# Kernel optimization log

Measured on AMD Instinct MI355X. Metric: run time of the kernel, lower is better.

## Reference

```python
import jax, jax.numpy as jnp
import numpy as np

EPS = 1e-3  # keras BatchNormalization default epsilon


def _dwconv_t(y, w):
    # depthwise conv along time (axis 1), SAME padding. y:(B,T,S,G,n), w:(G,n,k)
    k = w.shape[-1]
    T = y.shape[1]
    pl = (k - 1) // 2
    yp = jnp.pad(y, ((0, 0), (pl, k - 1 - pl), (0, 0), (0, 0), (0, 0)))
    return sum(yp[:, j:j + T] * w[..., j] for j in range(k))


def _tc_layer(x, w, b, k3, k5, k7, gamma, beta, mu, var):
    # x:(B,T,S,C); w:(5,G,Cg,nb); b/gamma/beta/mu/var:(5,G,nb); k*:(G,nb,k)
    B, T, S, C = x.shape
    G, nb = w.shape[1], w.shape[-1]
    # global spatial pooling: concat [x, max, mean] along spatial axis -> S+2
    x = jnp.concatenate([x, x.max(axis=2, keepdims=True), x.mean(axis=2, keepdims=True)], axis=2)
    S = S + 2
    xg = x.reshape(B, T, S, G, C // G)
    # 5 grouped 1x1x1 pointwise convs at once
    y = jnp.einsum('btsgc,pgcn->pbtsgn', xg, w) + b[:, None, None, None]
    t0 = y[0]
    t3 = _dwconv_t(y[1], k3)
    t5 = _dwconv_t(y[2], k5)
    t7 = _dwconv_t(y[3], k7)
    # temporal maxpool pool=2 stride=1 SAME (TF pads right)
    t1 = jnp.maximum(y[4], jnp.concatenate([y[4][:, 1:], y[4][:, -1:]], axis=1))
    ts = jnp.stack([t0, t3, t5, t7, t1])  # (5,B,T,S,G,nb)
    scale = gamma[:, None, None, None] / jnp.sqrt(var[:, None, None, None] + EPS)
    ts = (ts - mu[:, None, None, None]) * scale + beta[:, None, None, None]
    # concat branches within each group: (B,T,S,G,5*nb)
    z = jnp.transpose(ts, (1, 2, 3, 4, 0, 5)).reshape(B, T, S, G, 5 * nb)
    z = jax.nn.relu(z)
    # channel shuffle: (G, per) -> (per, G) -> flatten
    z = jnp.swapaxes(z, -1, -2).reshape(B, T, S, G * 5 * nb)
    # MaxPooling3D pool=(2,1,1) stride 2 valid: halve T
    return jnp.maximum(z[:, 0::2], z[:, 1::2])


def setup_inputs() -> dict:
    key = jax.random.key(0)
    ks = jax.random.split(key, 32)
    B, T, H, W, C = 16, 64, 7, 7, 1024
    G = 8
    d = {'x': jax.random.normal(ks[0], (B, T, H, W, C), jnp.float32)}
    specs = [(0, 128, 32), (1, 160, 40)]  # (layer, Cg, nb)
    i = 1
    for l, cg, nb in specs:
        d[f'w{l}'] = 0.02 * jax.random.normal(ks[i], (5, G, cg, nb)); i += 1
        d[f'b{l}'] = 0.02 * jax.random.normal(ks[i], (5, G, nb)); i += 1
        d[f'k3_{l}'] = 0.1 * jax.random.normal(ks[i], (G, nb, 3)); i += 1
        d[f'k5_{l}'] = 0.1 * jax.random.normal(ks[i], (G, nb, 5)); i += 1
        d[f'k7_{l}'] = 0.1 * jax.random.normal(ks[i], (G, nb, 7)); i += 1
        d[f'g{l}'] = jax.random.uniform(ks[i], (5, G, nb), minval=0.5, maxval=1.5); i += 1
        d[f'be{l}'] = 0.02 * jax.random.normal(ks[i], (5, G, nb)); i += 1
        d[f'mu{l}'] = 0.02 * jax.random.normal(ks[i], (5, G, nb)); i += 1
        d[f'v{l}'] = jax.random.uniform(ks[i], (5, G, nb), minval=0.5, maxval=1.5); i += 1
    return d


def reference(x, w0, b0, k3_0, k5_0, k7_0, g0, be0, mu0, v0,
              w1, b1, k3_1, k5_1, k7_1, g1, be1, mu1, v1):
    B, T, H, W, C = x.shape
    z = x.reshape(B, T, H * W, C)  # (B,T,S,C), side_dim2=1 kept implicit
    z = _tc_layer(z, w0, b0, k3_0, k5_0, k7_0, g0, be0, mu0, v0)
    z = _tc_layer(z, w1, b1, k3_1, k5_1, k7_1, g1, be1, mu1, v1)
    return z[:, :, :, None, :]  # (B, T/4, S+4, 1, Cout)
```

## Files before the change

kernel.cpp:

```cpp
#include <hip/hip_runtime.h>
#include <hip/hip_bf16.h>

#define EPSBN 1e-3f

typedef __attribute__((ext_vector_type(8))) short bf16x8;
typedef __attribute__((ext_vector_type(8))) unsigned short ushort8;
typedef __attribute__((ext_vector_type(4))) float f32x4;


__device__ __forceinline__ float bf2f(unsigned short u) {
    union { unsigned int i; float f; } c; c.i = (unsigned int)u << 16; return c.f;
}
__device__ __forceinline__ unsigned short f2bf(float f) {
    union { float f; unsigned int i; } c; c.f = f;
    unsigned int r = c.i + 0x7FFF + ((c.i >> 16) & 1);
    return (unsigned short)(r >> 16);
}

__global__ __launch_bounds__(256) void tc_prep(const float* __restrict__ w0,
                                               const float* __restrict__ w1,
                                               unsigned short* __restrict__ W0t,
                                               unsigned short* __restrict__ W1t) {
    const int idx = blockIdx.x * 256 + threadIdx.x;
    if (idx < 163840) {
        const int g   = idx / 20480;
        const int rem = idx - g*20480;
        const int n   = rem >> 7;
        const int k   = rem & 127;
        const int p   = n >> 5, nn = n & 31;
        W0t[idx] = f2bf(w0[(((size_t)p*8 + g)*128 + k)*32 + nn]);
    } else if (idx < 163840 + 256000) {
        const int i2  = idx - 163840;
        const int g   = i2 / 32000;
        const int rem = i2 - g*32000;
        const int n   = rem / 160;
        const int k   = rem - n*160;
        const int kref = (k % 20)*8 + k/20;
        const int p   = n / 40, nn = n - p*40;
        W1t[i2] = f2bf(w1[(((size_t)p*8 + g)*160 + kref)*40 + nn]);
    }
}

__global__ __launch_bounds__(256) void tc_reduce0(const float* __restrict__ x,
                                                  unsigned short* __restrict__ xb,
                                                  unsigned short* __restrict__ extb,
                                                  const int big) {
    const int bt = blockIdx.x;
    const int b  = bt >> 6, t = bt & 63;
    const int c  = threadIdx.x * 4;
    const float4* src = reinterpret_cast<const float4*>(x + (size_t)bt * 49 * 1024 + c);
    float4 v = src[0];
    float mx0 = v.x, mx1 = v.y, mx2 = v.z, mx3 = v.w;
    float sm0 = v.x, sm1 = v.y, sm2 = v.z, sm3 = v.w;
    if (big) {
        ushort4 o; o.x=f2bf(v.x); o.y=f2bf(v.y); o.z=f2bf(v.z); o.w=f2bf(v.w);
        *reinterpret_cast<ushort4*>(&xb[((size_t)(b*51)*64 + t)*1024 + c]) = o;
    }
    for (int s = 1; s < 49; ++s) {
        float4 u = src[(size_t)s * 256];
        mx0 = fmaxf(mx0, u.x); sm0 += u.x;
        mx1 = fmaxf(mx1, u.y); sm1 += u.y;
        mx2 = fmaxf(mx2, u.z); sm2 += u.z;
        mx3 = fmaxf(mx3, u.w); sm3 += u.w;
        if (big) {
            ushort4 o; o.x=f2bf(u.x); o.y=f2bf(u.y); o.z=f2bf(u.z); o.w=f2bf(u.w);
            *reinterpret_cast<ushort4*>(&xb[((size_t)(b*51 + s)*64 + t)*1024 + c]) = o;
        }
    }
    const float inv = 1.0f / 49.0f;
    ushort4 omx, omn;
    omx.x=f2bf(mx0); omx.y=f2bf(mx1); omx.z=f2bf(mx2); omx.w=f2bf(mx3);
    omn.x=f2bf(sm0*inv); omn.y=f2bf(sm1*inv); omn.z=f2bf(sm2*inv); omn.w=f2bf(sm3*inv);
    if (big) {
        *reinterpret_cast<ushort4*>(&xb[((size_t)(b*51 + 49)*64 + t)*1024 + c]) = omx;
        *reinterpret_cast<ushort4*>(&xb[((size_t)(b*51 + 50)*64 + t)*1024 + c]) = omn;
    } else {
        *reinterpret_cast<ushort4*>(&extb[((size_t)(b*2 + 0)*64 + t)*1024 + c]) = omx;
        *reinterpret_cast<ushort4*>(&extb[((size_t)(b*2 + 1)*64 + t)*1024 + c]) = omn;
    }
}

template<int BIG>
__global__ __launch_bounds__(512, 6) void tc_layer0(
    const float* __restrict__ x, const unsigned short* __restrict__ xb,
    const unsigned short* __restrict__ extb,
    const unsigned short* __restrict__ W0t, const float* __restrict__ bias,
    const float* __restrict__ k3, const float* __restrict__ k5,
    const float* __restrict__ k7,
    const float* __restrict__ gam, const float* __restrict__ bet,
    const float* __restrict__ mu, const float* __restrict__ var,
    unsigned short* __restrict__ zb)
{
    const int tid = threadIdx.x;
    const int g   = blockIdx.x / 416;
    const int rem = blockIdx.x % 416;
    const int sp  = rem % 26;
    const int b   = rem / 26;
    const int s0  = sp*2;
    const int has1 = (s0 + 1 < 51);

    __shared__ __align__(16) unsigned short lds[128*136 + 160*40];
    unsigned short* AtU = lds;
    unsigned short* WtU = lds + 128*136;
    unsigned short* Ytb = lds;

    #pragma unroll
    for (int it = 0; it < 4; ++it) {
        const int fid = tid + it*512;
        const int row = fid >> 4;
        const int ch8 = (fid & 15) * 8;
        const int t   = row & 63;
        const int s   = (row < 64) ? s0 : (has1 ? s0+1 : s0);
        ushort8 u;
        if (BIG) {
            u = *reinterpret_cast<const ushort8*>(
                &xb[((size_t)(b*51 + s)*64 + t)*1024 + g*128 + ch8]);
        } else if (s < 49) {
            const float* sp_ = x + ((size_t)(b*64 + t)*49 + s)*1024 + g*128 + ch8;
            const float4 f0 = *reinterpret_cast<const float4*>(sp_);
            const float4 f1 = *reinterpret_cast<const float4*>(sp_ + 4);
            u[0]=f2bf(f0.x); u[1]=f2bf(f0.y); u[2]=f2bf(f0.z); u[3]=f2bf(f0.w);
            u[4]=f2bf(f1.x); u[5]=f2bf(f1.y); u[6]=f2bf(f1.z); u[7]=f2bf(f1.w);
        } else {
            u = *reinterpret_cast<const ushort8*>(
                &extb[((size_t)(b*2 + (s-49))*64 + t)*1024 + g*128 + ch8]);
        }
        *reinterpret_cast<ushort8*>(&AtU[row*136 + ch8]) = u;
    }

    const int lane = tid & 63;
    const int wid  = tid >> 6;
    const int fr   = lane & 15;
    const int kb   = lane >> 4;

    f32x4 zero = {0.f, 0.f, 0.f, 0.f};
    f32x4 acc[10];
    #pragma unroll
    for (int i = 0; i < 10; ++i) acc[i] = zero;

    for (int kc = 0; kc < 4; ++kc) {
        __syncthreads();
        #pragma unroll
        for (int it = 0; it < 2; ++it) {
            const int gi = tid + it*512;
            if (gi < 640) {
                const int n = gi >> 2, part = (gi & 3) * 8;
                *reinterpret_cast<ushort8*>(&WtU[n*40 + part]) =
                    *reinterpret_cast<const ushort8*>(
                        &W0t[((size_t)g*160 + n)*128 + kc*32 + part]);
            }
        }
        __syncthreads();
        const bf16x8 bfrag = *reinterpret_cast<const bf16x8*>(
            &AtU[(wid*16 + fr)*136 + kc*32 + kb*8]);
        #pragma unroll
        for (int nt = 0; nt < 10; ++nt) {
            const bf16x8 afrag = *reinterpret_cast<const bf16x8*>(
                &WtU[(nt*16 + fr)*40 + kb*8]);
            acc[nt] = __builtin_amdgcn_mfma_f32_16x16x32_bf16(afrag, bfrag, acc[nt], 0, 0, 0);
        }
    }
    __syncthreads();
    #pragma unroll
    for (int nt = 0; nt < 10; ++nt)
        #pragma unroll
        for (int r = 0; r < 4; ++r)
            Ytb[(nt*16 + kb*4 + r)*134 + wid*16 + fr] = f2bf(acc[nt][r]);
    __syncthreads();

    if (tid < 320) {
        const int sIdx = (tid >= 160) ? 1 : 0;
        const int ch   = tid - sIdx*160;
        if (!sIdx || has1) {
            const int s  = s0 + sIdx;
            const int p  = ch >> 5, n = ch & 31;
            const int pi = (p*8 + g)*32 + n;
            const float bsv = bias[pi];
            const float sc  = gam[pi]*rsqrtf(var[pi]+EPSBN);
            const float sh  = bet[pi] - mu[pi]*sc;
            float yv[64];
            #pragma unroll
            for (int i = 0; i < 32; ++i) {
                const unsigned int w2 = *reinterpret_cast<const unsigned int*>(
                    &Ytb[ch*134 + sIdx*64 + i*2]);
                yv[2*i]   = bf2f((unsigned short)(w2 & 0xffffu)) + bsv;
                yv[2*i+1] = bf2f((unsigned short)(w2 >> 16)) + bsv;
            }
            unsigned short* zp = zb + ((size_t)(b*32)*53 + s)*1280 + g*160 + ch;
            if (p == 0) {
                #pragma unroll
                for (int tq = 0; tq < 32; ++tq) {
                    const float r = fmaxf(fmaxf(fmaf(yv[2*tq],sc,sh), fmaf(yv[2*tq+1],sc,sh)), 0.f);
                    zp[(size_t)tq*67840] = f2bf(r);
                }
            } else if (p == 1) {
                const float w0_ = k3[(g*32+n)*3+0], w1_ = k3[(g*32+n)*3+1], w2_ = k3[(g*32+n)*3+2];
                #pragma unroll
                for (int tq = 0; tq < 32; ++tq) {
                    float a = yv[2*tq]*w1_;
                    if (tq > 0) a = fmaf(yv[2*tq-1], w0_, a);
                    a = fmaf(yv[2*tq+1], w2_, a);
                    float c2 = fmaf(yv[2*tq], w0_, yv[2*tq+1]*w1_);
                    if (tq < 31) c2 = fmaf(yv[2*tq+2], w2_, c2);
                    const float r = fmaxf(fmaxf(fmaf(a,sc,sh), fmaf(c2,sc,sh)), 0.f);
                    zp[(size_t)tq*67840] = f2bf(r);
                }
            } else if (p == 2) {
                float wk[5];
                #pragma unroll
                for (int j = 0; j < 5; ++j) wk[j] = k5[(g*32+n)*5+j];
                #pragma unroll
                for (int tq = 0; tq < 32; ++tq) {
                    float vv[2];
                    #pragma unroll
                    for (int q = 0; q < 2; ++q) {
                        const int t = 2*tq + q;
                        float v = 0.f;
                        #pragma unroll
                        for (int j = 0; j < 5; ++j) {
                            const int ttp = t + j - 2;
                            if (ttp >= 0 && ttp < 64) v = fmaf(yv[ttp], wk[j], v);
                        }
                        vv[q] = v;
                    }
                    const float r = fmaxf(fmaxf(fmaf(vv[0],sc,sh), fmaf(vv[1],sc,sh)), 0.f);
                    zp[(size_t)tq*67840] = f2bf(r);
                }
            } else if (p == 3) {
                float wk[7];
                #pragma unroll
                for (int j = 0; j < 7; ++j) wk[j] = k7[(g*32+n)*7+j];
                #pragma unroll
                for (int tq = 0; tq < 32; ++tq) {
                    float vv[2];
                    #pragma unroll
                    for (int q = 0; q < 2; ++q) {
                        const int t = 2*tq + q;
                        float v = 0.f;
                        #pragma unroll
                        for (int j = 0; j < 7; ++j) {
                            const int ttp = t + j - 3;
                            if (ttp >= 0 && ttp < 64) v = fmaf(yv[ttp], wk[j], v);
                        }
                        vv[q] = v;
                    }
                    const float r = fmaxf(fmaxf(fmaf(vv[0],sc,sh), fmaf(vv[1],sc,sh)), 0.f);
                    zp[(size_t)tq*67840] = f2bf(r);
                }
            } else {
                #pragma unroll
                for (int tq = 0; tq < 32; ++tq) {
                    const float v0 = fmaxf(yv[2*tq], yv[2*tq+1]);
                    const float v1 = fmaxf(yv[2*tq+1], yv[(2*tq+2 < 64) ? 2*tq+2 : 63]);
                    const float r = fmaxf(fmaxf(fmaf(v0,sc,sh), fmaf(v1,sc,sh)), 0.f);
                    zp[(size_t)tq*67840] = f2bf(r);
                }
            }
        }
    }
}

__global__ __launch_bounds__(320) void tc_reduce1(unsigned short* __restrict__ zb) {
    const int bt = blockIdx.x;
    const int c  = threadIdx.x * 4;
    unsigned short* base = zb + (size_t)bt * 67840;
    ushort4 u = *reinterpret_cast<const ushort4*>(&base[c]);
    float v0 = bf2f(u.x), v1 = bf2f(u.y), v2 = bf2f(u.z), v3 = bf2f(u.w);
    float mx0 = v0, mx1 = v1, mx2 = v2, mx3 = v3;
    float sm0 = v0, sm1 = v1, sm2 = v2, sm3 = v3;
    for (int s = 1; s < 51; ++s) {
        ushort4 w = *reinterpret_cast<const ushort4*>(&base[(size_t)s*1280 + c]);
        v0 = bf2f(w.x); v1 = bf2f(w.y); v2 = bf2f(w.z); v3 = bf2f(w.w);
        mx0 = fmaxf(mx0, v0); sm0 += v0;
        mx1 = fmaxf(mx1, v1); sm1 += v1;
        mx2 = fmaxf(mx2, v2); sm2 += v2;
        mx3 = fmaxf(mx3, v3); sm3 += v3;
    }
    const float inv = 1.0f / 51.0f;
    ushort4 o;
    o.x = f2bf(mx0); o.y = f2bf(mx1); o.z = f2bf(mx2); o.w = f2bf(mx3);
    *reinterpret_cast<ushort4*>(&base[(size_t)51*1280 + c]) = o;
    o.x = f2bf(sm0*inv); o.y = f2bf(sm1*inv); o.z = f2bf(sm2*inv); o.w = f2bf(sm3*inv);
    *reinterpret_cast<ushort4*>(&base[(size_t)52*1280 + c]) = o;
}

__global__ __launch_bounds__(256, 4) void tc_layer1(
    const unsigned short* __restrict__ zbi,
    const unsigned short* __restrict__ W1t, const float* __restrict__ bias,
    const float* __restrict__ k3, const float* __restrict__ k5,
    const float* __restrict__ k7,
    const float* __restrict__ gam, const float* __restrict__ bet,
    const float* __restrict__ mu, const float* __restrict__ var,
    unsigned short* __restrict__ og)
{
    const int tid = threadIdx.x;
    const int g   = blockIdx.x / 432;
    const int rem = blockIdx.x % 432;
    const int sp  = rem % 27;
    const int b   = rem / 27;
    const int s0  = sp*2;
    const int has1 = (s0 + 1 < 53);

    __shared__ __align__(16) unsigned short lds[64*168 + 208*40];
    unsigned short* AtU = lds;
    unsigned short* WtU = lds + 64*168;
    unsigned short* Ytb = lds;

    if (tid < 40) {
        ushort8 z8 = {0,0,0,0,0,0,0,0};
        const int r = tid / 5, cp = tid - r*5;
        *reinterpret_cast<ushort8*>(&WtU[(200 + r)*40 + cp*8]) = z8;
    }

    #pragma unroll
    for (int it = 0; it < 10; ++it) {
        const int fid = tid + it*256;
        const int row = fid / 40;
        const int seg = fid - row*40;
        const int gg  = seg / 5, q = seg - gg*5;
        const int ch  = gg*160 + g*20 + q*4;
        const int s   = (row < 32) ? s0 : (has1 ? s0+1 : s0);
        const int t   = row & 31;
        const unsigned short* src = zbi + ((size_t)(b*32 + t)*53 + s)*1280 + ch;
        *reinterpret_cast<ushort4*>(&AtU[row*168 + seg*4]) =
            *reinterpret_cast<const ushort4*>(src);
    }

    const int lane = tid & 63;
    const int wid  = tid >> 6;
    const int fr   = lane & 15;
    const int kb   = lane >> 4;

    f32x4 zero = {0.f, 0.f, 0.f, 0.f};
    f32x4 acc[13];
    #pragma unroll
    for (int i = 0; i < 13; ++i) acc[i] = zero;

    for (int kc = 0; kc < 5; ++kc) {
        __syncthreads();
        #pragma unroll
        for (int it = 0; it < 4; ++it) {
            const int gi = tid + it*256;
            if (gi < 800) {
                const int n = gi >> 2, part = (gi & 3) * 8;
                *reinterpret_cast<ushort8*>(&WtU[n*40 + part]) =
                    *reinterpret_cast<const ushort8*>(
                        &W1t[((size_t)g*200 + n)*160 + kc*32 + part]);
            }
        }
        __syncthreads();
        const bf16x8 bfrag = *reinterpret_cast<const bf16x8*>(
            &AtU[(wid*16 + fr)*168 + kc*32 + kb*8]);
        #pragma unroll
        for (int nt = 0; nt < 13; ++nt) {
            const bf16x8 afrag = *reinterpret_cast<const bf16x8*>(
                &WtU[(nt*16 + fr)*40 + kb*8]);
            acc[nt] = __builtin_amdgcn_mfma_f32_16x16x32_bf16(afrag, bfrag, acc[nt], 0, 0, 0);
        }
    }
    __syncthreads();
    #pragma unroll
    for (int nt = 0; nt < 13; ++nt) {
        #pragma unroll
        for (int r = 0; r < 4; ++r) {
            const int n = nt*16 + kb*4 + r;
            if (n < 200) Ytb[n*70 + wid*16 + fr] = f2bf(acc[nt][r]);
        }
    }
    __syncthreads();

    #pragma unroll
    for (int it = 0; it < 2; ++it) {
        const int task = tid + it*256;
        if (task < 400) {
            const int sIdx = (task >= 200) ? 1 : 0;
            const int ch   = task - sIdx*200;
            if (sIdx && !has1) continue;
            const int s  = s0 + sIdx;
            const int p  = ch / 40, n = ch - p*40;
            const int pi = (p*8 + g)*40 + n;
            const float bsv = bias[pi];
            const float sc  = gam[pi]*rsqrtf(var[pi]+EPSBN);
            const float sh  = bet[pi] - mu[pi]*sc;
            float yv[32];
            #pragma unroll
            for (int i = 0; i < 16; ++i) {
                const unsigned int w2 = *reinterpret_cast<const unsigned int*>(
                    &Ytb[ch*70 + sIdx*32 + i*2]);
                yv[2*i]   = bf2f((unsigned short)(w2 & 0xffffu)) + bsv;
                yv[2*i+1] = bf2f((unsigned short)(w2 >> 16)) + bsv;
            }
            unsigned short* op = og + ((size_t)(b*16)*53 + s)*1600 + g*200 + ch;
            if (p == 0) {
                #pragma unroll
                for (int tq = 0; tq < 16; ++tq) {
                    const float r = fmaxf(fmaxf(fmaf(yv[2*tq],sc,sh), fmaf(yv[2*tq+1],sc,sh)), 0.f);
                    op[(size_t)tq*84800] = f2bf(r);
                }
            } else if (p == 1) {
                const float w0_ = k3[(g*40+n)*3+0], w1_ = k3[(g*40+n)*3+1], w2_ = k3[(g*40+n)*3+2];
                #pragma unroll
                for (int tq = 0; tq < 16; ++tq) {
                    float a = yv[2*tq]*w1_;
                    if (tq > 0) a = fmaf(yv[2*tq-1], w0_, a);
                    a = fmaf(yv[2*tq+1], w2_, a);
                    float c2 = fmaf(yv[2*tq], w0_, yv[2*tq+1]*w1_);
                    if (tq < 15) c2 = fmaf(yv[2*tq+2], w2_, c2);
                    const float r = fmaxf(fmaxf(fmaf(a,sc,sh), fmaf(c2,sc,sh)), 0.f);
                    op[(size_t)tq*84800] = f2bf(r);
                }
            } else if (p == 2) {
                float wk[5];
                #pragma unroll
                for (int j = 0; j < 5; ++j) wk[j] = k5[(g*40+n)*5+j];
                #pragma unroll
                for (int tq = 0; tq < 16; ++tq) {
                    float vv[2];
                    #pragma unroll
                    for (int q = 0; q < 2; ++q) {
                        const int t = 2*tq + q;
                        float v = 0.f;
                        #pragma unroll
                        for (int j = 0; j < 5; ++j) {
                            const int ttp = t + j - 2;
                            if (ttp >= 0 && ttp < 32) v = fmaf(yv[ttp], wk[j], v);
                        }
                        vv[q] = v;
                    }
                    const float r = fmaxf(fmaxf(fmaf(vv[0],sc,sh), fmaf(vv[1],sc,sh)), 0.f);
                    op[(size_t)tq*84800] = f2bf(r);
                }
            } else if (p == 3) {
                float wk[7];
                #pragma unroll
                for (int j = 0; j < 7; ++j) wk[j] = k7[(g*40+n)*7+j];
                #pragma unroll
                for (int tq = 0; tq < 16; ++tq) {
                    float vv[2];
                    #pragma unroll
                    for (int q = 0; q < 2; ++q) {
                        const int t = 2*tq + q;
                        float v = 0.f;
                        #pragma unroll
                        for (int j = 0; j < 7; ++j) {
                            const int ttp = t + j - 3;
                            if (ttp >= 0 && ttp < 32) v = fmaf(yv[ttp], wk[j], v);
                        }
                        vv[q] = v;
                    }
                    const float r = fmaxf(fmaxf(fmaf(vv[0],sc,sh), fmaf(vv[1],sc,sh)), 0.f);
                    op[(size_t)tq*84800] = f2bf(r);
                }
            } else {
                #pragma unroll
                for (int tq = 0; tq < 16; ++tq) {
                    const float v0 = fmaxf(yv[2*tq], yv[2*tq+1]);
                    const float v1 = fmaxf(yv[2*tq+1], yv[(2*tq+2 < 32) ? 2*tq+2 : 31]);
                    const float r = fmaxf(fmaxf(fmaf(v0,sc,sh), fmaf(v1,sc,sh)), 0.f);
                    op[(size_t)tq*84800] = f2bf(r);
                }
            }
        }
    }
}

__global__ __launch_bounds__(256) void tc_shuffle(const unsigned short* __restrict__ og,
                                                  float* __restrict__ o) {
    __shared__ unsigned short row[1600];
    const size_t base = (size_t)blockIdx.x * 1600;
    const int tid = threadIdx.x;
    if (tid < 200)
        *reinterpret_cast<ushort8*>(&row[tid*8]) =
            *reinterpret_cast<const ushort8*>(&og[base + (size_t)tid*8]);
    __syncthreads();
    #pragma unroll
    for (int it = 0; it < 2; ++it) {
        const int f4 = tid + it*256;
        if (f4 < 400) {
            const int c = f4*4;
            float4 v;
            v.x = bf2f(row[((c  ) & 7)*200 + ((c  ) >> 3)]);
            v.y = bf2f(row[((c+1) & 7)*200 + ((c+1) >> 3)]);
            v.z = bf2f(row[((c+2) & 7)*200 + ((c+2) >> 3)]);
            v.w = bf2f(row[((c+3) & 7)*200 + ((c+3) >> 3)]);
            *reinterpret_cast<float4*>(&o[base + (size_t)c]) = v;
        }
    }
}

extern "C" void kernel_launch(void* const* d_in, const int* in_sizes, int n_in,
                              void* d_out, int out_size, void* d_ws, size_t ws_size,
                              hipStream_t stream) {
    const float* x    = (const float*)d_in[0];
    const float* w0   = (const float*)d_in[1];
    const float* b0   = (const float*)d_in[2];
    const float* k3_0 = (const float*)d_in[3];
    const float* k5_0 = (const float*)d_in[4];
    const float* k7_0 = (const float*)d_in[5];
    const float* g0   = (const float*)d_in[6];
    const float* be0  = (const float*)d_in[7];
    const float* mu0  = (const float*)d_in[8];
    const float* v0   = (const float*)d_in[9];
    const float* w1   = (const float*)d_in[10];
    const float* b1   = (const float*)d_in[11];
    const float* k3_1 = (const float*)d_in[12];
    const float* k5_1 = (const float*)d_in[13];
    const float* k7_1 = (const float*)d_in[14];
    const float* g1   = (const float*)d_in[15];
    const float* be1  = (const float*)d_in[16];
    const float* mu1  = (const float*)d_in[17];
    const float* v1   = (const float*)d_in[18];

    const size_t n_zb   = 34734080;
    const size_t n_W0t  = 163840;
    const size_t n_W1t  = 256000;
    const size_t n_extb = 2097152;
    const size_t n_og   = 21708800;
    const size_t n_xb   = 53477376;

    unsigned short* zb   = (unsigned short*)d_ws;
    unsigned short* W0t  = zb + n_zb;
    unsigned short* W1t  = W0t + n_W0t;
    unsigned short* extb = W1t + n_W1t;
    unsigned short* og   = extb + n_extb;
    unsigned short* xb   = og + n_og;
    const size_t need_big = (n_zb + n_W0t + n_W1t + n_extb + n_og + n_xb) * 2;
    const int big = (ws_size >= need_big) ? 1 : 0;

    tc_prep   <<<1640, 256, 0, stream>>>(w0, w1, W0t, W1t);
    tc_reduce0<<<16*64, 256, 0, stream>>>(x, xb, extb, big);
    if (big)
        tc_layer0<1><<<416*8, 512, 0, stream>>>(x, xb, extb, W0t, b0, k3_0, k5_0,
                                                k7_0, g0, be0, mu0, v0, zb);
    else
        tc_layer0<0><<<416*8, 512, 0, stream>>>(x, xb, extb, W0t, b0, k3_0, k5_0,
                                                k7_0, g0, be0, mu0, v0, zb);
    tc_reduce1<<<16*32, 320, 0, stream>>>(zb);
    tc_layer1 <<<432*8, 256, 0, stream>>>(zb, W1t, b1, k3_1, k5_1, k7_1,
                                          g1, be1, mu1, v1, og);
    tc_shuffle<<<16*16*53, 256, 0, stream>>>(og, (float*)d_out);
}
```

Before: 266.3 us.

## Drop bf16 staging copy of input and widen layer1 tiles to four spatial slices

Removes the big-workspace path, where tc_reduce0 wrote a bf16 copy of the whole input and layer0 read it. Layer0 now always converts the fp32 input inline, saving a large extra write and read. Layer1 now processes four spatial positions per 512-thread block instead of two per 256-thread block, so each block amortises the W1t weight-chunk loads over twice as many rows. The cost is more LDS per block and possibly lower occupancy, and layer0's launch bound drops from 6 to 4 waves per SIMD.

Measured after the change: 256.2 us. 3.8% less time.

```diff
diff --git a/kernel.cpp b/kernel.cpp
--- a/kernel.cpp
+++ b/kernel.cpp
@@ -42,9 +42,7 @@
 }
 
 __global__ __launch_bounds__(256) void tc_reduce0(const float* __restrict__ x,
-                                                  unsigned short* __restrict__ xb,
-                                                  unsigned short* __restrict__ extb,
-                                                  const int big) {
+                                                  unsigned short* __restrict__ extb) {
     const int bt = blockIdx.x;
     const int b  = bt >> 6, t = bt & 63;
     const int c  = threadIdx.x * 4;
@@ -52,38 +50,23 @@
     float4 v = src[0];
     float mx0 = v.x, mx1 = v.y, mx2 = v.z, mx3 = v.w;
     float sm0 = v.x, sm1 = v.y, sm2 = v.z, sm3 = v.w;
-    if (big) {
-        ushort4 o; o.x=f2bf(v.x); o.y=f2bf(v.y); o.z=f2bf(v.z); o.w=f2bf(v.w);
-        *reinterpret_cast<ushort4*>(&xb[((size_t)(b*51)*64 + t)*1024 + c]) = o;
-    }
     for (int s = 1; s < 49; ++s) {
         float4 u = src[(size_t)s * 256];
         mx0 = fmaxf(mx0, u.x); sm0 += u.x;
         mx1 = fmaxf(mx1, u.y); sm1 += u.y;
         mx2 = fmaxf(mx2, u.z); sm2 += u.z;
         mx3 = fmaxf(mx3, u.w); sm3 += u.w;
-        if (big) {
-            ushort4 o; o.x=f2bf(u.x); o.y=f2bf(u.y); o.z=f2bf(u.z); o.w=f2bf(u.w);
-            *reinterpret_cast<ushort4*>(&xb[((size_t)(b*51 + s)*64 + t)*1024 + c]) = o;
-        }
     }
     const float inv = 1.0f / 49.0f;
     ushort4 omx, omn;
     omx.x=f2bf(mx0); omx.y=f2bf(mx1); omx.z=f2bf(mx2); omx.w=f2bf(mx3);
     omn.x=f2bf(sm0*inv); omn.y=f2bf(sm1*inv); omn.z=f2bf(sm2*inv); omn.w=f2bf(sm3*inv);
-    if (big) {
-        *reinterpret_cast<ushort4*>(&xb[((size_t)(b*51 + 49)*64 + t)*1024 + c]) = omx;
-        *reinterpret_cast<ushort4*>(&xb[((size_t)(b*51 + 50)*64 + t)*1024 + c]) = omn;
-    } else {
-        *reinterpret_cast<ushort4*>(&extb[((size_t)(b*2 + 0)*64 + t)*1024 + c]) = omx;
-        *reinterpret_cast<ushort4*>(&extb[((size_t)(b*2 + 1)*64 + t)*1024 + c]) = omn;
-    }
-}
-
-template<int BIG>
-__global__ __launch_bounds__(512, 6) void tc_layer0(
-    const float* __restrict__ x, const unsigned short* __restrict__ xb,
-    const unsigned short* __restrict__ extb,
+    *reinterpret_cast<ushort4*>(&extb[((size_t)(b*2 + 0)*64 + t)*1024 + c]) = omx;
+    *reinterpret_cast<ushort4*>(&extb[((size_t)(b*2 + 1)*64 + t)*1024 + c]) = omn;
+}
+
+__global__ __launch_bounds__(512, 4) void tc_layer0(
+    const float* __restrict__ x, const unsigned short* __restrict__ extb,
     const unsigned short* __restrict__ W0t, const float* __restrict__ bias,
     const float* __restrict__ k3, const float* __restrict__ k5,
     const float* __restrict__ k7,
@@ -112,10 +95,7 @@
         const int t   = row & 63;
         const int s   = (row < 64) ? s0 : (has1 ? s0+1 : s0);
         ushort8 u;
-        if (BIG) {
-            u = *reinterpret_cast<const ushort8*>(
-                &xb[((size_t)(b*51 + s)*64 + t)*1024 + g*128 + ch8]);
-        } else if (s < 49) {
+        if (s < 49) {
             const float* sp_ = x + ((size_t)(b*64 + t)*49 + s)*1024 + g*128 + ch8;
             const float4 f0 = *reinterpret_cast<const float4*>(sp_);
             const float4 f1 = *reinterpret_cast<const float4*>(sp_ + 4);
@@ -284,7 +264,7 @@
     *reinterpret_cast<ushort4*>(&base[(size_t)52*1280 + c]) = o;
 }
 
-__global__ __launch_bounds__(256, 4) void tc_layer1(
+__global__ __launch_bounds__(512, 4) void tc_layer1(
     const unsigned short* __restrict__ zbi,
     const unsigned short* __restrict__ W1t, const float* __restrict__ bias,
     const float* __restrict__ k3, const float* __restrict__ k5,
@@ -294,16 +274,16 @@
     unsigned short* __restrict__ og)
 {
     const int tid = threadIdx.x;
-    const int g   = blockIdx.x / 432;
-    const int rem = blockIdx.x % 432;
-    const int sp  = rem % 27;
-    const int b   = rem / 27;
-    const int s0  = sp*2;
-    const int has1 = (s0 + 1 < 53);
-
-    __shared__ __align__(16) unsigned short lds[64*168 + 208*40];
+    const int g   = blockIdx.x / 224;
+    const int rem = blockIdx.x % 224;
+    const int sq  = rem % 14;
+    const int b   = rem / 14;
+    const int s0  = sq*4;
+    const int ns  = (53 - s0 < 4) ? (53 - s0) : 4;
+
+    __shared__ __align__(16) unsigned short lds[128*168 + 208*40];
     unsigned short* AtU = lds;
-    unsigned short* WtU = lds + 64*168;
+    unsigned short* WtU = lds + 128*168;
     unsigned short* Ytb = lds;
 
     if (tid < 40) {
@@ -314,12 +294,13 @@
 
     #pragma unroll
     for (int it = 0; it < 10; ++it) {
-        const int fid = tid + it*256;
+        const int fid = tid + it*512;
         const int row = fid / 40;
         const int seg = fid - row*40;
         const int gg  = seg / 5, q = seg - gg*5;
         const int ch  = gg*160 + g*20 + q*4;
-        const int s   = (row < 32) ? s0 : (has1 ? s0+1 : s0);
+        const int sl  = row >> 5;
+        const int s   = s0 + ((sl < ns) ? sl : 0);
         const int t   = row & 31;
         const unsigned short* src = zbi + ((size_t)(b*32 + t)*53 + s)*1280 + ch;
         *reinterpret_cast<ushort4*>(&AtU[row*168 + seg*4]) =
@@ -339,8 +320,8 @@
     for (int kc = 0; kc < 5; ++kc) {
         __syncthreads();
         #pragma unroll
-        for (int it = 0; it < 4; ++it) {
-            const int gi = tid + it*256;
+        for (int it = 0; it < 2; ++it) {
+            const int gi = tid + it*512;
             if (gi < 800) {
                 const int n = gi >> 2, part = (gi & 3) * 8;
                 *reinterpret_cast<ushort8*>(&WtU[n*40 + part]) =
@@ -364,100 +345,101 @@
         #pragma unroll
         for (int r = 0; r < 4; ++r) {
             const int n = nt*16 + kb*4 + r;
-            if (n < 200) Ytb[n*70 + wid*16 + fr] = f2bf(acc[nt][r]);
+            if (n < 200) Ytb[n*134 + wid*16 + fr] = f2bf(acc[nt][r]);
         }
     }
     __syncthreads();
 
     #pragma unroll
     for (int it = 0; it < 2; ++it) {
-        const int task = tid + it*256;
-        if (task < 400) {
-            const int sIdx = (task >= 200) ? 1 : 0;
+        const int task = tid + it*512;
+        if (task < 800) {
+            const int sIdx = task / 200;
             const int ch   = task - sIdx*200;
-            if (sIdx && !has1) continue;
-            const int s  = s0 + sIdx;
-            const int p  = ch / 40, n = ch - p*40;
-            const int pi = (p*8 + g)*40 + n;
-            const float bsv = bias[pi];
-            const float sc  = gam[pi]*rsqrtf(var[pi]+EPSBN);
-            const float sh  = bet[pi] - mu[pi]*sc;
-            float yv[32];
-            #pragma unroll
-            for (int i = 0; i < 16; ++i) {
-                const unsigned int w2 = *reinterpret_cast<const unsigned int*>(
-                    &Ytb[ch*70 + sIdx*32 + i*2]);
-                yv[2*i]   = bf2f((unsigned short)(w2 & 0xffffu)) + bsv;
-                yv[2*i+1] = bf2f((unsigned short)(w2 >> 16)) + bsv;
-            }
-            unsigned short* op = og + ((size_t)(b*16)*53 + s)*1600 + g*200 + ch;
-            if (p == 0) {
-                #pragma unroll
-                for (int tq = 0; tq < 16; ++tq) {
-                    const float r = fmaxf(fmaxf(fmaf(yv[2*tq],sc,sh), fmaf(yv[2*tq+1],sc,sh)), 0.f);
-                    op[(size_t)tq*84800] = f2bf(r);
-                }
-            } else if (p == 1) {
-                const float w0_ = k3[(g*40+n)*3+0], w1_ = k3[(g*40+n)*3+1], w2_ = k3[(g*40+n)*3+2];
-                #pragma unroll
-                for (int tq = 0; tq < 16; ++tq) {
-                    float a = yv[2*tq]*w1_;
-                    if (tq > 0) a = fmaf(yv[2*tq-1], w0_, a);
-                    a = fmaf(yv[2*tq+1], w2_, a);
-                    float c2 = fmaf(yv[2*tq], w0_, yv[2*tq+1]*w1_);
-                    if (tq < 15) c2 = fmaf(yv[2*tq+2], w2_, c2);
-                    const float r = fmaxf(fmaxf(fmaf(a,sc,sh), fmaf(c2,sc,sh)), 0.f);
-                    op[(size_t)tq*84800] = f2bf(r);
-                }
-            } else if (p == 2) {
-                float wk[5];
-                #pragma unroll
-                for (int j = 0; j < 5; ++j) wk[j] = k5[(g*40+n)*5+j];
-                #pragma unroll
-                for (int tq = 0; tq < 16; ++tq) {
-                    float vv[2];
-                    #pragma unroll
-                    for (int q = 0; q < 2; ++q) {
-                        const int t = 2*tq + q;
-                        float v = 0.f;
+            if (sIdx < ns) {
+                const int s  = s0 + sIdx;
+                const int p  = ch / 40, n = ch - p*40;
+                const int pi = (p*8 + g)*40 + n;
+                const float bsv = bias[pi];
+                const float sc  = gam[pi]*rsqrtf(var[pi]+EPSBN);
+                const float sh  = bet[pi] - mu[pi]*sc;
+                float yv[32];
+                #pragma unroll
+                for (int i = 0; i < 16; ++i) {
+                    const unsigned int w2 = *reinterpret_cast<const unsigned int*>(
+                        &Ytb[ch*134 + sIdx*32 + i*2]);
+                    yv[2*i]   = bf2f((unsigned short)(w2 & 0xffffu)) + bsv;
+                    yv[2*i+1] = bf2f((unsigned short)(w2 >> 16)) + bsv;
+                }
+                unsigned short* op = og + ((size_t)(b*16)*53 + s)*1600 + g*200 + ch;
+                if (p == 0) {
+                    #pragma unroll
+                    for (int tq = 0; tq < 16; ++tq) {
+                        const float r = fmaxf(fmaxf(fmaf(yv[2*tq],sc,sh), fmaf(yv[2*tq+1],sc,sh)), 0.f);
+                        op[(size_t)tq*84800] = f2bf(r);
+                    }
+                } else if (p == 1) {
+                    const float w0_ = k3[(g*40+n)*3+0], w1_ = k3[(g*40+n)*3+1], w2_ = k3[(g*40+n)*3+2];
+                    #pragma unroll
+                    for (int tq = 0; tq < 16; ++tq) {
+                        float a = yv[2*tq]*w1_;
+                        if (tq > 0) a = fmaf(yv[2*tq-1], w0_, a);
+                        a = fmaf(yv[2*tq+1], w2_, a);
+                        float c2 = fmaf(yv[2*tq], w0_, yv[2*tq+1]*w1_);
+                        if (tq < 15) c2 = fmaf(yv[2*tq+2], w2_, c2);
+                        const float r = fmaxf(fmaxf(fmaf(a,sc,sh), fmaf(c2,sc,sh)), 0.f);
+                        op[(size_t)tq*84800] = f2bf(r);
+                    }
+                } else if (p == 2) {
+                    float wk[5];
+                    #pragma unroll
+                    for (int j = 0; j < 5; ++j) wk[j] = k5[(g*40+n)*5+j];
+                    #pragma unroll
+                    for (int tq = 0; tq < 16; ++tq) {
+                        float vv[2];
                         #pragma unroll
-                        for (int j = 0; j < 5; ++j) {
-                            const int ttp = t + j - 2;
-                            if (ttp >= 0 && ttp < 32) v = fmaf(yv[ttp], wk[j], v);
+                        for (int q = 0; q < 2; ++q) {
+                            const int t = 2*tq + q;
+                            float v = 0.f;
+                            #pragma unroll
+                            for (int j = 0; j < 5; ++j) {
+                                const int ttp = t + j - 2;
+                                if (ttp >= 0 && ttp < 32) v = fmaf(yv[ttp], wk[j], v);
+                            }
+                            vv[q] = v;
                         }
-                        vv[q] = v;
-                    }
-                    const float r = fmaxf(fmaxf(fmaf(vv[0],sc,sh), fmaf(vv[1],sc,sh)), 0.f);
-                    op[(size_t)tq*84800] = f2bf(r);
-                }
-            } else if (p == 3) {
-                float wk[7];
-                #pragma unroll
-                for (int j = 0; j < 7; ++j) wk[j] = k7[(g*40+n)*7+j];
-                #pragma unroll
-                for (int tq = 0; tq < 16; ++tq) {
-                    float vv[2];
-                    #pragma unroll
-                    for (int q = 0; q < 2; ++q) {
-                        const int t = 2*tq + q;
-                        float v = 0.f;
+                        const float r = fmaxf(fmaxf(fmaf(vv[0],sc,sh), fmaf(vv[1],sc,sh)), 0.f);
+                        op[(size_t)tq*84800] = f2bf(r);
+                    }
+                } else if (p == 3) {
+                    float wk[7];
+                    #pragma unroll
+                    for (int j = 0; j < 7; ++j) wk[j] = k7[(g*40+n)*7+j];
+                    #pragma unroll
+                    for (int tq = 0; tq < 16; ++tq) {
+                        float vv[2];
                         #pragma unroll
-                        for (int j = 0; j < 7; ++j) {
-                            const int ttp = t + j - 3;
-                            if (ttp >= 0 && ttp < 32) v = fmaf(yv[ttp], wk[j], v);
+                        for (int q = 0; q < 2; ++q) {
+                            const int t = 2*tq + q;
+                            float v = 0.f;
+                            #pragma unroll
+                            for (int j = 0; j < 7; ++j) {
+                                const int ttp = t + j - 3;
+                                if (ttp >= 0 && ttp < 32) v = fmaf(yv[ttp], wk[j], v);
+                            }
+                            vv[q] = v;
                         }
-                        vv[q] = v;
-                    }
-                    const float r = fmaxf(fmaxf(fmaf(vv[0],sc,sh), fmaf(vv[1],sc,sh)), 0.f);
-                    op[(size_t)tq*84800] = f2bf(r);
-                }
-            } else {
-                #pragma unroll
-                for (int tq = 0; tq < 16; ++tq) {
-                    const float v0 = fmaxf(yv[2*tq], yv[2*tq+1]);
-                    const float v1 = fmaxf(yv[2*tq+1], yv[(2*tq+2 < 32) ? 2*tq+2 : 31]);
-                    const float r = fmaxf(fmaxf(fmaf(v0,sc,sh), fmaf(v1,sc,sh)), 0.f);
-                    op[(size_t)tq*84800] = f2bf(r);
+                        const float r = fmaxf(fmaxf(fmaf(vv[0],sc,sh), fmaf(vv[1],sc,sh)), 0.f);
+                        op[(size_t)tq*84800] = f2bf(r);
+                    }
+                } else {
+                    #pragma unroll
+                    for (int tq = 0; tq < 16; ++tq) {
+                        const float v0 = fmaxf(yv[2*tq], yv[2*tq+1]);
+                        const float v1 = fmaxf(yv[2*tq+1], yv[(2*tq+2 < 32) ? 2*tq+2 : 31]);
+                        const float r = fmaxf(fmaxf(fmaf(v0,sc,sh), fmaf(v1,sc,sh)), 0.f);
+                        op[(size_t)tq*84800] = f2bf(r);
+                    }
                 }
             }
         }
@@ -515,28 +497,19 @@
     const size_t n_W0t  = 163840;
     const size_t n_W1t  = 256000;
     const size_t n_extb = 2097152;
-    const size_t n_og   = 21708800;
-    const size_t n_xb   = 53477376;
 
     unsigned short* zb   = (unsigned short*)d_ws;
     unsigned short* W0t  = zb + n_zb;
     unsigned short* W1t  = W0t + n_W0t;
     unsigned short* extb = W1t + n_W1t;
     unsigned short* og   = extb + n_extb;
-    unsigned short* xb   = og + n_og;
-    const size_t need_big = (n_zb + n_W0t + n_W1t + n_extb + n_og + n_xb) * 2;
-    const int big = (ws_size >= need_big) ? 1 : 0;
 
     tc_prep   <<<1640, 256, 0, stream>>>(w0, w1, W0t, W1t);
-    tc_reduce0<<<16*64, 256, 0, stream>>>(x, xb, extb, big);
-    if (big)
-        tc_layer0<1><<<416*8, 512, 0, stream>>>(x, xb, extb, W0t, b0, k3_0, k5_0,
-                                                k7_0, g0, be0, mu0, v0, zb);
-    else
-        tc_layer0<0><<<416*8, 512, 0, stream>>>(x, xb, extb, W0t, b0, k3_0, k5_0,
-                                                k7_0, g0, be0, mu0, v0, zb);
+    tc_reduce0<<<16*64, 256, 0, stream>>>(x, extb);
+    tc_layer0 <<<416*8, 512, 0, stream>>>(x, extb, W0t, b0, k3_0, k5_0,
+                                          k7_0, g0, be0, mu0, v0, zb);
     tc_reduce1<<<16*32, 320, 0, stream>>>(zb);
-    tc_layer1 <<<432*8, 256, 0, stream>>>(zb, W1t, b1, k3_1, k5_1, k7_1,
+    tc_layer1 <<<224*8, 512, 0, stream>>>(zb, W1t, b1, k3_1, k5_1, k7_1,
                                           g1, be1, mu1, v1, og);
     tc_shuffle<<<16*16*53, 256, 0, stream>>>(og, (float*)d_out);
 }
```
